# Performance work log

Hardware: AMD Instinct MI355X
Metric: run time of the kernel (lower is better)

Reference implementation:

```python
import jax, jax.numpy as jnp
import numpy as np

B, D, L, R, O = 32768, 128, 3, 64, 64
EPS = 1e-5


def setup_inputs() -> dict:
    key = jax.random.key(0)
    ks = jax.random.split(key, 5)
    s_in = 1.0 / np.sqrt(D)
    s_r = 1.0 / np.sqrt(R)
    return {
        "x": jax.random.normal(ks[0], (B, D, L), dtype=jnp.float32),
        "layer0": jax.random.uniform(ks[1], (D, R), minval=-s_in, maxval=s_in, dtype=jnp.float32),
        "core1": jax.random.uniform(ks[2], (R, D, R), minval=-s_in, maxval=s_in, dtype=jnp.float32),
        "core2": jax.random.uniform(ks[3], (R, D, R), minval=-s_in, maxval=s_in, dtype=jnp.float32),
        "last": jax.random.uniform(ks[4], (R, O), minval=-s_r, maxval=s_r, dtype=jnp.float32),
        "ln_w": jnp.ones((D, L), dtype=jnp.float32),
        "ln_b": jnp.zeros((D, L), dtype=jnp.float32),
    }


def reference(x, layer0, core1, core2, last, ln_w, ln_b):
    # LayerNorm over the last two dims [D, L] with affine params
    mu = jnp.mean(x, axis=(1, 2), keepdims=True)
    var = jnp.var(x, axis=(1, 2), keepdims=True)
    xn = (x - mu) * jax.lax.rsqrt(var + EPS) * ln_w + ln_b  # [B, D, L]

    # Tensor-train contraction chain. The original builds a khatri-rao
    # [B, R*D] per step then matmuls with the reshaped [R*D, R] core;
    # einsum 'br,bd,rds->bs' computes the identical contraction fused.
    temp = xn[:, :, 0] @ layer0  # [B, R]
    temp = jnp.einsum("br,bd,rds->bs", temp, xn[:, :, 1], core1)
    temp = jnp.einsum("br,bd,rds->bs", temp, xn[:, :, 2], core2)
    return temp @ last  # [B, O]
```

## Files before the change

kernel.cpp:

```cpp
#include <hip/hip_runtime.h>
#include <hip/hip_fp16.h>

typedef _Float16 f16x8 __attribute__((ext_vector_type(8)));
typedef float f32x16 __attribute__((ext_vector_type(16)));

union H2x4 { f16x8 v; __half2 h2[4]; unsigned u[4]; };
union U1H2 { unsigned u; __half2 h; };

#define TB 128
#define SLOT0_OFF 0
#define SLOT1_OFF 32768
#define T_OFF     65536
#define XN12_OFF  81920
#define SMEM_BYTES 148480
#define WS_CT1   0
#define WS_CT2   1048576
#define WS_L0T   2097152
#define WS_LASTT 2113536

#define WAITBAR0() asm volatile("s_waitcnt vmcnt(0)\n\ts_barrier" ::: "memory")

__device__ __forceinline__ void gload_lds16(const void* g, void* l) {
  __builtin_amdgcn_global_load_lds(
      (const __attribute__((address_space(1))) unsigned int*)g,
      (__attribute__((address_space(3))) unsigned int*)l, 16, 0, 0);
}

__device__ __forceinline__ void issue_chunk32(const unsigned char* g,
                                              unsigned char* l, int tid) {
  gload_lds16(g + tid * 16, l + tid * 16);
  gload_lds16(g + tid * 16 + 16384, l + tid * 16 + 16384);
}

__device__ __forceinline__ unsigned pack_h2(float a, float b) {
  return (unsigned)__half_as_ushort(__float2half(a)) |
         ((unsigned)__half_as_ushort(__float2half(b)) << 16);
}

__device__ __forceinline__ void reduce_T(unsigned char* smem, f32x16 a0, f32x16 a1,
                                         int p, int kh, int mh, int h, int scol) {
  float* scr = (float*)(smem + (kh ? SLOT1_OFF : SLOT0_OFF));
  __syncthreads();
  if (p == 0) {
#pragma unroll
    for (int j = 0; j < 16; ++j) {
      const int r0 = (j & 3) + 8 * (j >> 2) + 4 * h;
      const int row = mh * 64 + r0;
      scr[row * 64 + scol] = a0[j];
      scr[(row + 32) * 64 + scol] = a1[j];
    }
  }
  __syncthreads();
  if (p == 1) {
#pragma unroll
    for (int j = 0; j < 16; ++j) {
      const int r0 = (j & 3) + 8 * (j >> 2) + 4 * h;
      const int row = mh * 64 + r0;
      scr[row * 64 + scol] += a0[j];
      scr[(row + 32) * 64 + scol] += a1[j];
    }
  }
  __syncthreads();
  if (p == 0) {
    const float* s0 = (const float*)(smem + SLOT0_OFF);
    const float* s1 = (const float*)(smem + SLOT1_OFF);
#pragma unroll
    for (int j = 0; j < 16; ++j) {
      const int r0 = (j & 3) + 8 * (j >> 2) + 4 * h;
      const int row = mh * 64 + kh * 32 + r0;
      const float vsum = s0[row * 64 + scol] + s1[row * 64 + scol];
      *(__half*)(smem + T_OFF + row * 128 + ((2 * scol) ^ ((row & 7) << 4))) =
          __float2half(vsum);
    }
  }
  __syncthreads();
}

__global__ void __launch_bounds__(512) tt_prep(
    const float* __restrict__ layer0, const float* __restrict__ core1,
    const float* __restrict__ core2, const float* __restrict__ last,
    unsigned char* __restrict__ ws) {
  const int tid = blockIdx.x * 512 + threadIdx.x;
  if (tid < 524288) {
    const int which = tid >> 18;
    const int w = tid & 262143;
    const float* core = which ? core2 : core1;
    unsigned char* ct = ws + (which ? WS_CT2 : WS_CT1);
    const int j   = w & 3;
    const int lp  = (w >> 2) & 63;
    const int blk = w >> 8;
    const int kbL = blk & 1;
    const int kh  = (blk >> 1) & 1;
    const int sb  = (blk >> 2) & 1;
    const int d   = blk >> 3;
    const int hh  = lp & 1;
    const int l31 = lp >> 1;
    const int s   = sb * 32 + l31;
    const int r0  = kh * 32 + kbL * 16 + hh * 8 + 2 * j;
    const unsigned val = pack_h2(core[r0 * 8192 + d * 64 + s],
                                 core[(r0 + 1) * 8192 + d * 64 + s]);
    *(unsigned*)(ct + (size_t)w * 4) = val;
  } else if (tid < 528384) {
    const int w = tid - 524288;
    const int r = w >> 6, j = w & 63, d = 2 * j;
    const unsigned val = pack_h2(layer0[d * 64 + r], layer0[(d + 1) * 64 + r]);
    *(unsigned*)(ws + WS_L0T + r * 256 + 4 * j) = val;
  } else if (tid < 530432) {
    const int w = tid - 528384;
    const int o = w >> 5, j = w & 31, r = 2 * j;
    const unsigned val = pack_h2(last[r * 64 + o], last[(r + 1) * 64 + o]);
    *(unsigned*)(ws + WS_LASTT + o * 128 + 4 * j) = val;
  }
}

__global__ void __launch_bounds__(1024, 4) tt_fused(
    const float* __restrict__ x, const float* __restrict__ lnw,
    const float* __restrict__ lnb, const unsigned char* __restrict__ ws,
    float* __restrict__ out) {
  __shared__ alignas(16) unsigned char smem[SMEM_BYTES];
  const int tid = threadIdx.x;
  const int wid = tid >> 6;
  const int lane = tid & 63;
  const int l31 = lane & 31;
  const int h = lane >> 5;
  const int p  = wid & 1;
  const int kh = (wid >> 1) & 1;
  const int sb = (wid >> 2) & 1;
  const int mh = (wid >> 3) & 1;
  const int bg0 = blockIdx.x * TB;
  const int scol = sb * 32 + l31;
  const int lp16 = (l31 * 2 + h) * 16;
  const int swzA = (l31 & 7) << 4;

  {
    float wv[6], bv[6];
#pragma unroll
    for (int k = 0; k < 6; ++k) { wv[k] = lnw[lane + 64 * k]; bv[k] = lnb[lane + 64 * k]; }
#pragma unroll
    for (int rr = 0; rr < 8; ++rr) {
      const int row = wid * 8 + rr;
      const float* xrow = x + (size_t)(bg0 + row) * 384;
      float v[6];
#pragma unroll
      for (int k = 0; k < 6; ++k) v[k] = xrow[lane + 64 * k];
      float s = 0.f, ss = 0.f;
#pragma unroll
      for (int k = 0; k < 6; ++k) { s += v[k]; ss += v[k] * v[k]; }
#pragma unroll
      for (int m = 1; m < 64; m <<= 1) { s += __shfl_xor(s, m); ss += __shfl_xor(ss, m); }
      const float mu = s * (1.f / 384.f);
      const float var = ss * (1.f / 384.f) - mu * mu;
      const float rstd = rsqrtf(var + 1e-5f);
#pragma unroll
      for (int k = 0; k < 6; ++k) {
        const int i = lane + 64 * k;
        const int d = i / 3;
        const int sl = i - 3 * d;
        const float xv = (v[k] - mu) * rstd * wv[k] + bv[k];
        if (sl == 0) {
          *(__half*)(smem + SLOT0_OFF + row * 256 + ((2 * d) ^ ((row & 7) << 4))) =
              __float2half(xv);
        } else {
          *(__half*)(smem + XN12_OFF + d * 520 + 4 * row + 2 * (sl - 1)) =
              __float2half(xv);
        }
      }
    }
  }
  __syncthreads();

  f32x16 acc0, acc1;

#pragma unroll
  for (int i = 0; i < 16; ++i) { acc0[i] = 0.f; acc1[i] = 0.f; }
  {
    const unsigned char* l0t = ws + WS_L0T;
#pragma unroll
    for (int kbL = 0; kbL < 2; ++kbL) {
      const int cb = (((p << 1) | kh) * 2 + kbL) * 32 + h * 16;
      f16x8 bf = *(const f16x8*)(l0t + scol * 256 + cb);
      f16x8 a0 = *(const f16x8*)(smem + SLOT0_OFF + (mh * 64 + l31) * 256 + (cb ^ swzA));
      f16x8 a1 = *(const f16x8*)(smem + SLOT0_OFF + (mh * 64 + 32 + l31) * 256 + (cb ^ swzA));
      acc0 = __builtin_amdgcn_mfma_f32_32x32x16_f16(a0, bf, acc0, 0, 0, 0);
      acc1 = __builtin_amdgcn_mfma_f32_32x32x16_f16(a1, bf, acc1, 0, 0, 0);
    }
  }
  reduce_T(smem, acc0, acc1, p, kh, mh, h, scol);

  for (int st = 0; st < 2; ++st) {
    const unsigned char* ctg = ws + (st ? WS_CT2 : WS_CT1);

    issue_chunk32(ctg, smem + SLOT0_OFF, tid);

    H2x4 tp00, tp01, tp10, tp11;
    {
      const int rb0 = kh * 64 + h * 16;
      const int ra = (mh * 64 + l31) * 128;
      const int rb = (mh * 64 + 32 + l31) * 128;
      tp00.v = *(const f16x8*)(smem + T_OFF + ra + (rb0 ^ swzA));
      tp01.v = *(const f16x8*)(smem + T_OFF + ra + ((rb0 + 32) ^ swzA));
      tp10.v = *(const f16x8*)(smem + T_OFF + rb + (rb0 ^ swzA));
      tp11.v = *(const f16x8*)(smem + T_OFF + rb + ((rb0 + 32) ^ swzA));
    }

#pragma unroll
    for (int i = 0; i < 16; ++i) { acc0[i] = 0.f; acc1[i] = 0.f; }

#pragma unroll 1
    for (int cg = 0; cg < 32; ++cg) {
      WAITBAR0();
      if (cg < 31)
        issue_chunk32(ctg + (cg + 1) * 32768,
                      smem + ((cg + 1) & 1) * 32768, tid);
      const unsigned char* chunk = smem + (cg & 1) * 32768;
#pragma unroll
      for (int dh = 0; dh < 2; ++dh) {
        const int dloc = p + 2 * dh;
        const unsigned char* bp = chunk + dloc * 8192 + sb * 4096 + kh * 2048 + lp16;
        f16x8 bf0 = *(const f16x8*)(bp);
        f16x8 bf1 = *(const f16x8*)(bp + 1024);
        const unsigned char* xp = smem + XN12_OFF + (4 * cg + dloc) * 520 +
                                  4 * (mh * 64 + l31) + 2 * st;
        const unsigned xv0 = *(const unsigned short*)xp;
        const unsigned xv1 = *(const unsigned short*)(xp + 128);
        U1H2 e0, e1;
        e0.u = xv0 | (xv0 << 16);
        e1.u = xv1 | (xv1 << 16);
        {
          H2x4 af0, af1;
#pragma unroll
          for (int q = 0; q < 4; ++q) {
            af0.h2[q] = __hmul2(tp00.h2[q], e0.h);
            af1.h2[q] = __hmul2(tp10.h2[q], e1.h);
          }
          acc0 = __builtin_amdgcn_mfma_f32_32x32x16_f16(af0.v, bf0, acc0, 0, 0, 0);
          acc1 = __builtin_amdgcn_mfma_f32_32x32x16_f16(af1.v, bf0, acc1, 0, 0, 0);
        }
        {
          H2x4 af0, af1;
#pragma unroll
          for (int q = 0; q < 4; ++q) {
            af0.h2[q] = __hmul2(tp01.h2[q], e0.h);
            af1.h2[q] = __hmul2(tp11.h2[q], e1.h);
          }
          acc0 = __builtin_amdgcn_mfma_f32_32x32x16_f16(af0.v, bf1, acc0, 0, 0, 0);
          acc1 = __builtin_amdgcn_mfma_f32_32x32x16_f16(af1.v, bf1, acc1, 0, 0, 0);
        }
      }
    }
    reduce_T(smem, acc0, acc1, p, kh, mh, h, scol);
  }

  if (p == 0) {
    f32x16 accd;
#pragma unroll
    for (int i = 0; i < 16; ++i) accd[i] = 0.f;
    const unsigned char* lastT = ws + WS_LASTT;
    const int rbase = mh * 64 + kh * 32;
#pragma unroll
    for (int kb = 0; kb < 4; ++kb) {
      const int cb = kb * 32 + h * 16;
      f16x8 bf = *(const f16x8*)(lastT + scol * 128 + cb);
      f16x8 af = *(const f16x8*)(smem + T_OFF + (rbase + l31) * 128 + (cb ^ swzA));
      accd = __builtin_amdgcn_mfma_f32_32x32x16_f16(af, bf, accd, 0, 0, 0);
    }
#pragma unroll
    for (int j = 0; j < 16; ++j) {
      const int r0 = (j & 3) + 8 * (j >> 2) + 4 * h;
      out[(size_t)(bg0 + rbase + r0) * 64 + scol] = accd[j];
    }
  }
}

extern "C" void kernel_launch(void* const* d_in, const int* in_sizes, int n_in,
                              void* d_out, int out_size, void* d_ws, size_t ws_size,
                              hipStream_t stream) {
  const float* x      = (const float*)d_in[0];
  const float* layer0 = (const float*)d_in[1];
  const float* core1  = (const float*)d_in[2];
  const float* core2  = (const float*)d_in[3];
  const float* last   = (const float*)d_in[4];
  const float* lnw    = (const float*)d_in[5];
  const float* lnb    = (const float*)d_in[6];
  unsigned char* ws   = (unsigned char*)d_ws;
  float* outp         = (float*)d_out;

  tt_prep<<<1036, 512, 0, stream>>>(layer0, core1, core2, last, ws);
  tt_fused<<<256, 1024, 0, stream>>>(x, lnw, lnb, ws, outp);
}
```

Measured before the change: 98.58 us.

## Replace double-buffered core chunks with 4-slot 16KB ring, prefetch depth 3

The core-tensor streaming loop now uses a four-slot ring of 16KB chunks instead of two 32KB buffers. Each iteration waits only until the current chunk has landed (vmcnt(2)), so up to three chunk loads stay in flight. Each iteration handles two d values instead of four, so the loop runs 64 times instead of 32. This should hide more global-to-LDS latency, at the cost of twice as many barriers per stage.

```diff
diff --git a/kernel.cpp b/kernel.cpp
--- a/kernel.cpp
+++ b/kernel.cpp
@@ -8,8 +8,7 @@
 union U1H2 { unsigned u; __half2 h; };
 
 #define TB 128
-#define SLOT0_OFF 0
-#define SLOT1_OFF 32768
+#define RING_OFF  0
 #define T_OFF     65536
 #define XN12_OFF  81920
 #define SMEM_BYTES 148480
@@ -18,7 +17,7 @@
 #define WS_L0T   2097152
 #define WS_LASTT 2113536
 
-#define WAITBAR0() asm volatile("s_waitcnt vmcnt(0)\n\ts_barrier" ::: "memory")
+#define WAITBAR(N) asm volatile("s_waitcnt vmcnt(" #N ")\n\ts_barrier" ::: "memory")
 
 __device__ __forceinline__ void gload_lds16(const void* g, void* l) {
   __builtin_amdgcn_global_load_lds(
@@ -26,10 +25,9 @@
       (__attribute__((address_space(3))) unsigned int*)l, 16, 0, 0);
 }
 
-__device__ __forceinline__ void issue_chunk32(const unsigned char* g,
+__device__ __forceinline__ void issue_chunk16(const unsigned char* g,
                                               unsigned char* l, int tid) {
   gload_lds16(g + tid * 16, l + tid * 16);
-  gload_lds16(g + tid * 16 + 16384, l + tid * 16 + 16384);
 }
 
 __device__ __forceinline__ unsigned pack_h2(float a, float b) {
@@ -39,7 +37,7 @@
 
 __device__ __forceinline__ void reduce_T(unsigned char* smem, f32x16 a0, f32x16 a1,
                                          int p, int kh, int mh, int h, int scol) {
-  float* scr = (float*)(smem + (kh ? SLOT1_OFF : SLOT0_OFF));
+  float* scr = (float*)(smem + RING_OFF + kh * 32768);
   __syncthreads();
   if (p == 0) {
 #pragma unroll
@@ -62,8 +60,8 @@
   }
   __syncthreads();
   if (p == 0) {
-    const float* s0 = (const float*)(smem + SLOT0_OFF);
-    const float* s1 = (const float*)(smem + SLOT1_OFF);
+    const float* s0 = (const float*)(smem + RING_OFF);
+    const float* s1 = (const float*)(smem + RING_OFF + 32768);
 #pragma unroll
     for (int j = 0; j < 16; ++j) {
       const int r0 = (j & 3) + 8 * (j >> 2) + 4 * h;
@@ -158,7 +156,7 @@
         const int sl = i - 3 * d;
         const float xv = (v[k] - mu) * rstd * wv[k] + bv[k];
         if (sl == 0) {
-          *(__half*)(smem + SLOT0_OFF + row * 256 + ((2 * d) ^ ((row & 7) << 4))) =
+          *(__half*)(smem + RING_OFF + row * 256 + ((2 * d) ^ ((row & 7) << 4))) =
               __float2half(xv);
         } else {
           *(__half*)(smem + XN12_OFF + d * 520 + 4 * row + 2 * (sl - 1)) =
@@ -179,8 +177,8 @@
     for (int kbL = 0; kbL < 2; ++kbL) {
       const int cb = (((p << 1) | kh) * 2 + kbL) * 32 + h * 16;
       f16x8 bf = *(const f16x8*)(l0t + scol * 256 + cb);
-      f16x8 a0 = *(const f16x8*)(smem + SLOT0_OFF + (mh * 64 + l31) * 256 + (cb ^ swzA));
-      f16x8 a1 = *(const f16x8*)(smem + SLOT0_OFF + (mh * 64 + 32 + l31) * 256 + (cb ^ swzA));
+      f16x8 a0 = *(const f16x8*)(smem + RING_OFF + (mh * 64 + l31) * 256 + (cb ^ swzA));
+      f16x8 a1 = *(const f16x8*)(smem + RING_OFF + (mh * 64 + 32 + l31) * 256 + (cb ^ swzA));
       acc0 = __builtin_amdgcn_mfma_f32_32x32x16_f16(a0, bf, acc0, 0, 0, 0);
       acc1 = __builtin_amdgcn_mfma_f32_32x32x16_f16(a1, bf, acc1, 0, 0, 0);
     }
@@ -190,7 +188,9 @@
   for (int st = 0; st < 2; ++st) {
     const unsigned char* ctg = ws + (st ? WS_CT2 : WS_CT1);
 
-    issue_chunk32(ctg, smem + SLOT0_OFF, tid);
+    issue_chunk16(ctg,         smem + RING_OFF,         tid);
+    issue_chunk16(ctg + 16384, smem + RING_OFF + 16384, tid);
+    issue_chunk16(ctg + 32768, smem + RING_OFF + 32768, tid);
 
     H2x4 tp00, tp01, tp10, tp11;
     {
@@ -207,45 +207,43 @@
     for (int i = 0; i < 16; ++i) { acc0[i] = 0.f; acc1[i] = 0.f; }
 
 #pragma unroll 1
-    for (int cg = 0; cg < 32; ++cg) {
-      WAITBAR0();
-      if (cg < 31)
-        issue_chunk32(ctg + (cg + 1) * 32768,
-                      smem + ((cg + 1) & 1) * 32768, tid);
-      const unsigned char* chunk = smem + (cg & 1) * 32768;
-#pragma unroll
-      for (int dh = 0; dh < 2; ++dh) {
-        const int dloc = p + 2 * dh;
-        const unsigned char* bp = chunk + dloc * 8192 + sb * 4096 + kh * 2048 + lp16;
-        f16x8 bf0 = *(const f16x8*)(bp);
-        f16x8 bf1 = *(const f16x8*)(bp + 1024);
-        const unsigned char* xp = smem + XN12_OFF + (4 * cg + dloc) * 520 +
-                                  4 * (mh * 64 + l31) + 2 * st;
-        const unsigned xv0 = *(const unsigned short*)xp;
-        const unsigned xv1 = *(const unsigned short*)(xp + 128);
-        U1H2 e0, e1;
-        e0.u = xv0 | (xv0 << 16);
-        e1.u = xv1 | (xv1 << 16);
-        {
-          H2x4 af0, af1;
-#pragma unroll
-          for (int q = 0; q < 4; ++q) {
-            af0.h2[q] = __hmul2(tp00.h2[q], e0.h);
-            af1.h2[q] = __hmul2(tp10.h2[q], e1.h);
-          }
-          acc0 = __builtin_amdgcn_mfma_f32_32x32x16_f16(af0.v, bf0, acc0, 0, 0, 0);
-          acc1 = __builtin_amdgcn_mfma_f32_32x32x16_f16(af1.v, bf0, acc1, 0, 0, 0);
+    for (int cg = 0; cg < 64; ++cg) {
+      if (cg <= 61)      WAITBAR(2);
+      else if (cg == 62) WAITBAR(1);
+      else               WAITBAR(0);
+      if (cg < 61)
+        issue_chunk16(ctg + (cg + 3) * 16384,
+                      smem + RING_OFF + ((cg + 3) & 3) * 16384, tid);
+      const unsigned char* bp = smem + RING_OFF + (cg & 3) * 16384 +
+                                p * 8192 + sb * 4096 + kh * 2048 + lp16;
+      f16x8 bf0 = *(const f16x8*)(bp);
+      f16x8 bf1 = *(const f16x8*)(bp + 1024);
+      const unsigned char* xp = smem + XN12_OFF + (2 * cg + p) * 520 +
+                                4 * (mh * 64 + l31) + 2 * st;
+      const unsigned xv0 = *(const unsigned short*)xp;
+      const unsigned xv1 = *(const unsigned short*)(xp + 128);
+      U1H2 e0, e1;
+      e0.u = xv0 | (xv0 << 16);
+      e1.u = xv1 | (xv1 << 16);
+      {
+        H2x4 af0, af1;
+#pragma unroll
+        for (int q = 0; q < 4; ++q) {
+          af0.h2[q] = __hmul2(tp00.h2[q], e0.h);
+          af1.h2[q] = __hmul2(tp10.h2[q], e1.h);
         }
-        {
-          H2x4 af0, af1;
-#pragma unroll
-          for (int q = 0; q < 4; ++q) {
-            af0.h2[q] = __hmul2(tp01.h2[q], e0.h);
-            af1.h2[q] = __hmul2(tp11.h2[q], e1.h);
-          }
-          acc0 = __builtin_amdgcn_mfma_f32_32x32x16_f16(af0.v, bf1, acc0, 0, 0, 0);
-          acc1 = __builtin_amdgcn_mfma_f32_32x32x16_f16(af1.v, bf1, acc1, 0, 0, 0);
+        acc0 = __builtin_amdgcn_mfma_f32_32x32x16_f16(af0.v, bf0, acc0, 0, 0, 0);
+        acc1 = __builtin_amdgcn_mfma_f32_32x32x16_f16(af1.v, bf0, acc1, 0, 0, 0);
+      }
+      {
+        H2x4 af0, af1;
+#pragma unroll
+        for (int q = 0; q < 4; ++q) {
+          af0.h2[q] = __hmul2(tp01.h2[q], e0.h);
+          af1.h2[q] = __hmul2(tp11.h2[q], e1.h);
         }
+        acc0 = __builtin_amdgcn_mfma_f32_32x32x16_f16(af0.v, bf1, acc0, 0, 0, 0);
+        acc1 = __builtin_amdgcn_mfma_f32_32x32x16_f16(af1.v, bf1, acc1, 0, 0, 0);
       }
     }
     reduce_T(smem, acc0, acc1, p, kh, mh, h, scol);
```

After: 102.3 us. 1.04x slower.

## Halve batch tile to 64 rows with 512-thread blocks and 16KB core chunks

Applied to the files above, without the earlier changes.

The batch tile per block drops from 128 to 64 rows, and the block size from 1024 to 512 threads by removing the mh split. The streamed core chunks shrink to 16KB, covering two d values per step over 64 steps instead of four over 32. Shared memory is halved, which should allow two blocks per CU and better overlap across blocks. In exchange, each core byte is reused by half as many rows, doubling total core traffic from L2, and the number of barriers per stage doubles.

```diff
diff --git a/kernel.cpp b/kernel.cpp
--- a/kernel.cpp
+++ b/kernel.cpp
@@ -7,12 +7,12 @@
 union H2x4 { f16x8 v; __half2 h2[4]; unsigned u[4]; };
 union U1H2 { unsigned u; __half2 h; };
 
-#define TB 128
+#define TB 64
 #define SLOT0_OFF 0
-#define SLOT1_OFF 32768
-#define T_OFF     65536
-#define XN12_OFF  81920
-#define SMEM_BYTES 148480
+#define SLOT1_OFF 16384
+#define T_OFF     32768
+#define XN12_OFF  40960
+#define SMEM_BYTES 74752
 #define WS_CT1   0
 #define WS_CT2   1048576
 #define WS_L0T   2097152
@@ -26,10 +26,10 @@
       (__attribute__((address_space(3))) unsigned int*)l, 16, 0, 0);
 }
 
-__device__ __forceinline__ void issue_chunk32(const unsigned char* g,
+__device__ __forceinline__ void issue_chunk16(const unsigned char* g,
                                               unsigned char* l, int tid) {
   gload_lds16(g + tid * 16, l + tid * 16);
-  gload_lds16(g + tid * 16 + 16384, l + tid * 16 + 16384);
+  gload_lds16(g + tid * 16 + 8192, l + tid * 16 + 8192);
 }
 
 __device__ __forceinline__ unsigned pack_h2(float a, float b) {
@@ -38,16 +38,15 @@
 }
 
 __device__ __forceinline__ void reduce_T(unsigned char* smem, f32x16 a0, f32x16 a1,
-                                         int p, int kh, int mh, int h, int scol) {
+                                         int p, int kh, int h, int scol) {
   float* scr = (float*)(smem + (kh ? SLOT1_OFF : SLOT0_OFF));
   __syncthreads();
   if (p == 0) {
 #pragma unroll
     for (int j = 0; j < 16; ++j) {
       const int r0 = (j & 3) + 8 * (j >> 2) + 4 * h;
-      const int row = mh * 64 + r0;
-      scr[row * 64 + scol] = a0[j];
-      scr[(row + 32) * 64 + scol] = a1[j];
+      scr[r0 * 64 + scol] = a0[j];
+      scr[(32 + r0) * 64 + scol] = a1[j];
     }
   }
   __syncthreads();
@@ -55,9 +54,8 @@
 #pragma unroll
     for (int j = 0; j < 16; ++j) {
       const int r0 = (j & 3) + 8 * (j >> 2) + 4 * h;
-      const int row = mh * 64 + r0;
-      scr[row * 64 + scol] += a0[j];
-      scr[(row + 32) * 64 + scol] += a1[j];
+      scr[r0 * 64 + scol] += a0[j];
+      scr[(32 + r0) * 64 + scol] += a1[j];
     }
   }
   __syncthreads();
@@ -67,7 +65,7 @@
 #pragma unroll
     for (int j = 0; j < 16; ++j) {
       const int r0 = (j & 3) + 8 * (j >> 2) + 4 * h;
-      const int row = mh * 64 + kh * 32 + r0;
+      const int row = kh * 32 + r0;
       const float vsum = s0[row * 64 + scol] + s1[row * 64 + scol];
       *(__half*)(smem + T_OFF + row * 128 + ((2 * scol) ^ ((row & 7) << 4))) =
           __float2half(vsum);
@@ -113,7 +111,7 @@
   }
 }
 
-__global__ void __launch_bounds__(1024, 4) tt_fused(
+__global__ void __launch_bounds__(512, 4) tt_fused(
     const float* __restrict__ x, const float* __restrict__ lnw,
     const float* __restrict__ lnb, const unsigned char* __restrict__ ws,
     float* __restrict__ out) {
@@ -126,7 +124,6 @@
   const int p  = wid & 1;
   const int kh = (wid >> 1) & 1;
   const int sb = (wid >> 2) & 1;
-  const int mh = (wid >> 3) & 1;
   const int bg0 = blockIdx.x * TB;
   const int scol = sb * 32 + l31;
   const int lp16 = (l31 * 2 + h) * 16;
@@ -161,7 +158,7 @@
           *(__half*)(smem + SLOT0_OFF + row * 256 + ((2 * d) ^ ((row & 7) << 4))) =
               __float2half(xv);
         } else {
-          *(__half*)(smem + XN12_OFF + d * 520 + 4 * row + 2 * (sl - 1)) =
+          *(__half*)(smem + XN12_OFF + d * 264 + 4 * row + 2 * (sl - 1)) =
               __float2half(xv);
         }
       }
@@ -179,76 +176,72 @@
     for (int kbL = 0; kbL < 2; ++kbL) {
       const int cb = (((p << 1) | kh) * 2 + kbL) * 32 + h * 16;
       f16x8 bf = *(const f16x8*)(l0t + scol * 256 + cb);
-      f16x8 a0 = *(const f16x8*)(smem + SLOT0_OFF + (mh * 64 + l31) * 256 + (cb ^ swzA));
-      f16x8 a1 = *(const f16x8*)(smem + SLOT0_OFF + (mh * 64 + 32 + l31) * 256 + (cb ^ swzA));
+      f16x8 a0 = *(const f16x8*)(smem + SLOT0_OFF + l31 * 256 + (cb ^ swzA));
+      f16x8 a1 = *(const f16x8*)(smem + SLOT0_OFF + (32 + l31) * 256 + (cb ^ swzA));
       acc0 = __builtin_amdgcn_mfma_f32_32x32x16_f16(a0, bf, acc0, 0, 0, 0);
       acc1 = __builtin_amdgcn_mfma_f32_32x32x16_f16(a1, bf, acc1, 0, 0, 0);
     }
   }
-  reduce_T(smem, acc0, acc1, p, kh, mh, h, scol);
+  reduce_T(smem, acc0, acc1, p, kh, h, scol);
 
   for (int st = 0; st < 2; ++st) {
     const unsigned char* ctg = ws + (st ? WS_CT2 : WS_CT1);
 
-    issue_chunk32(ctg, smem + SLOT0_OFF, tid);
+    issue_chunk16(ctg, smem + SLOT0_OFF, tid);
 
     H2x4 tp00, tp01, tp10, tp11;
     {
       const int rb0 = kh * 64 + h * 16;
-      const int ra = (mh * 64 + l31) * 128;
-      const int rb = (mh * 64 + 32 + l31) * 128;
-      tp00.v = *(const f16x8*)(smem + T_OFF + ra + (rb0 ^ swzA));
-      tp01.v = *(const f16x8*)(smem + T_OFF + ra + ((rb0 + 32) ^ swzA));
-      tp10.v = *(const f16x8*)(smem + T_OFF + rb + (rb0 ^ swzA));
-      tp11.v = *(const f16x8*)(smem + T_OFF + rb + ((rb0 + 32) ^ swzA));
+      tp00.v = *(const f16x8*)(smem + T_OFF + l31 * 128 + (rb0 ^ swzA));
+      tp01.v = *(const f16x8*)(smem + T_OFF + l31 * 128 + ((rb0 + 32) ^ swzA));
+      tp10.v = *(const f16x8*)(smem + T_OFF + (32 + l31) * 128 + (rb0 ^ swzA));
+      tp11.v = *(const f16x8*)(smem + T_OFF + (32 + l31) * 128 + ((rb0 + 32) ^ swzA));
     }
 
 #pragma unroll
     for (int i = 0; i < 16; ++i) { acc0[i] = 0.f; acc1[i] = 0.f; }
 
 #pragma unroll 1
-    for (int cg = 0; cg < 32; ++cg) {
-      WAITBAR0();
-      if (cg < 31)
-        issue_chunk32(ctg + (cg + 1) * 32768,
-                      smem + ((cg + 1) & 1) * 32768, tid);
-      const unsigned char* chunk = smem + (cg & 1) * 32768;
-#pragma unroll
-      for (int dh = 0; dh < 2; ++dh) {
-        const int dloc = p + 2 * dh;
-        const unsigned char* bp = chunk + dloc * 8192 + sb * 4096 + kh * 2048 + lp16;
-        f16x8 bf0 = *(const f16x8*)(bp);
-        f16x8 bf1 = *(const f16x8*)(bp + 1024);
-        const unsigned char* xp = smem + XN12_OFF + (4 * cg + dloc) * 520 +
-                                  4 * (mh * 64 + l31) + 2 * st;
+    for (int cg = 0; cg < 64; ++cg) {
+      U1H2 e0, e1;
+      {
+        const unsigned char* xp = smem + XN12_OFF + (2 * cg + p) * 264 +
+                                  4 * l31 + 2 * st;
         const unsigned xv0 = *(const unsigned short*)xp;
         const unsigned xv1 = *(const unsigned short*)(xp + 128);
-        U1H2 e0, e1;
         e0.u = xv0 | (xv0 << 16);
         e1.u = xv1 | (xv1 << 16);
-        {
-          H2x4 af0, af1;
-#pragma unroll
-          for (int q = 0; q < 4; ++q) {
-            af0.h2[q] = __hmul2(tp00.h2[q], e0.h);
-            af1.h2[q] = __hmul2(tp10.h2[q], e1.h);
-          }
-          acc0 = __builtin_amdgcn_mfma_f32_32x32x16_f16(af0.v, bf0, acc0, 0, 0, 0);
-          acc1 = __builtin_amdgcn_mfma_f32_32x32x16_f16(af1.v, bf0, acc1, 0, 0, 0);
+      }
+      WAITBAR0();
+      if (cg < 63)
+        issue_chunk16(ctg + (cg + 1) * 16384,
+                      smem + ((cg + 1) & 1) * 16384, tid);
+      const unsigned char* bp = smem + (cg & 1) * 16384 +
+                                p * 8192 + sb * 4096 + kh * 2048 + lp16;
+      f16x8 bf0 = *(const f16x8*)(bp);
+      f16x8 bf1 = *(const f16x8*)(bp + 1024);
+      {
+        H2x4 af0, af1;
+#pragma unroll
+        for (int q = 0; q < 4; ++q) {
+          af0.h2[q] = __hmul2(tp00.h2[q], e0.h);
+          af1.h2[q] = __hmul2(tp10.h2[q], e1.h);
         }
-        {
-          H2x4 af0, af1;
-#pragma unroll
-          for (int q = 0; q < 4; ++q) {
-            af0.h2[q] = __hmul2(tp01.h2[q], e0.h);
-            af1.h2[q] = __hmul2(tp11.h2[q], e1.h);
-          }
-          acc0 = __builtin_amdgcn_mfma_f32_32x32x16_f16(af0.v, bf1, acc0, 0, 0, 0);
-          acc1 = __builtin_amdgcn_mfma_f32_32x32x16_f16(af1.v, bf1, acc1, 0, 0, 0);
+        acc0 = __builtin_amdgcn_mfma_f32_32x32x16_f16(af0.v, bf0, acc0, 0, 0, 0);
+        acc1 = __builtin_amdgcn_mfma_f32_32x32x16_f16(af1.v, bf0, acc1, 0, 0, 0);
+      }
+      {
+        H2x4 af0, af1;
+#pragma unroll
+        for (int q = 0; q < 4; ++q) {
+          af0.h2[q] = __hmul2(tp01.h2[q], e0.h);
+          af1.h2[q] = __hmul2(tp11.h2[q], e1.h);
         }
-      }
-    }
-    reduce_T(smem, acc0, acc1, p, kh, mh, h, scol);
+        acc0 = __builtin_amdgcn_mfma_f32_32x32x16_f16(af0.v, bf1, acc0, 0, 0, 0);
+        acc1 = __builtin_amdgcn_mfma_f32_32x32x16_f16(af1.v, bf1, acc1, 0, 0, 0);
+      }
+    }
+    reduce_T(smem, acc0, acc1, p, kh, h, scol);
   }
 
   if (p == 0) {
@@ -256,18 +249,17 @@
 #pragma unroll
     for (int i = 0; i < 16; ++i) accd[i] = 0.f;
     const unsigned char* lastT = ws + WS_LASTT;
-    const int rbase = mh * 64 + kh * 32;
 #pragma unroll
     for (int kb = 0; kb < 4; ++kb) {
       const int cb = kb * 32 + h * 16;
       f16x8 bf = *(const f16x8*)(lastT + scol * 128 + cb);
-      f16x8 af = *(const f16x8*)(smem + T_OFF + (rbase + l31) * 128 + (cb ^ swzA));
+      f16x8 af = *(const f16x8*)(smem + T_OFF + (kh * 32 + l31) * 128 + (cb ^ swzA));
       accd = __builtin_amdgcn_mfma_f32_32x32x16_f16(af, bf, accd, 0, 0, 0);
     }
 #pragma unroll
     for (int j = 0; j < 16; ++j) {
       const int r0 = (j & 3) + 8 * (j >> 2) + 4 * h;
-      out[(size_t)(bg0 + rbase + r0) * 64 + scol] = accd[j];
+      out[(size_t)(bg0 + kh * 32 + r0) * 64 + scol] = accd[j];
     }
   }
 }
@@ -286,5 +278,5 @@
   float* outp         = (float*)d_out;
 
   tt_prep<<<1036, 512, 0, stream>>>(layer0, core1, core2, last, ws);
-  tt_fused<<<256, 1024, 0, stream>>>(x, lnw, lnb, ws, outp);
-}
+  tt_fused<<<512, 512, 0, stream>>>(x, lnw, lnb, ws, outp);
+}
```

Result: slower. 107.2 us (+8.8%).
